# Kernel optimization log

Hardware: AMD Instinct MI355X
Metric: run time of the kernel (lower is better)

Reference implementation:

```python
import jax, jax.numpy as jnp
import numpy as np

N, IN, OUT, RANK = 8192, 4096, 4096, 16
SCALING = 2.0

def setup_inputs() -> dict:
    key = jax.random.key(0)
    k1, k2, k3, k4 = jax.random.split(key, 4)
    x = jax.random.normal(k1, (N, IN), dtype=jnp.float32)
    weight = jax.random.normal(k2, (OUT, IN), dtype=jnp.float32) * (1.0 / np.sqrt(IN))
    lora_A = jax.random.normal(k3, (RANK, IN), dtype=jnp.float32) * (1.0 / np.sqrt(IN))
    lora_B = jax.random.normal(k4, (OUT, RANK), dtype=jnp.float32) * 0.01
    return {"x": x, "weight": weight, "lora_A": lora_A, "lora_B": lora_B}

def reference(x, weight, lora_A, lora_B):
    # frozen base linear: F.linear(x, weight) == x @ weight.T  -> [N, OUT]
    base = jnp.einsum('ni,oi->no', x, weight)
    # LoRA branch: dropout(x) (p=0 => identity) @ A.T @ B.T, scaled
    lora = jnp.einsum('ni,ri->nr', x, lora_A)      # [N, RANK]
    lora = jnp.einsum('nr,or->no', lora, lora_B)   # [N, OUT]
    return base + lora * SCALING
```

## Files before the change

### kernel.cpp

```cpp
#include <hip/hip_runtime.h>


#define N_ROWS 8192
#define K_DIM  4096
#define N_COLS 4096
#define RANK   16
#define BK     64
#define NT     (K_DIM / BK)

#define XBLK ((N_ROWS * K_DIM / 4) / 256)
#define WBLK ((N_COLS * K_DIM / 4) / 256)

typedef __bf16 bf16x8 __attribute__((ext_vector_type(8)));
typedef float  f32x4  __attribute__((ext_vector_type(4)));

__device__ __forceinline__ unsigned short f2bf(float f) {
  unsigned int u = __builtin_bit_cast(unsigned int, f);
  u += 0x7FFFu + ((u >> 16) & 1u);
  return (unsigned short)(u >> 16);
}


__global__ __launch_bounds__(256) void prep_kernel(const float* __restrict__ x,
                                                   const float* __restrict__ w,
                                                   const float* __restrict__ A,
                                                   const float* __restrict__ Bm,
                                                   unsigned short* __restrict__ xb,
                                                   unsigned short* __restrict__ wb) {
  const int b = blockIdx.x;
  if (b < XBLK) {
    size_t idx = (size_t)b * 256 + threadIdx.x;
    const float4 v = *reinterpret_cast<const float4*>(x + idx * 4);
    ushort4 r;
    r.x = f2bf(v.x); r.y = f2bf(v.y); r.z = f2bf(v.z); r.w = f2bf(v.w);
    *reinterpret_cast<ushort4*>(xb + idx * 4) = r;
  } else {
    size_t idx = (size_t)(b - XBLK) * 256 + threadIdx.x;
    int o  = (int)(idx >> 10);
    int ic = (int)(idx & 1023) << 2;
    const float4 wv = *reinterpret_cast<const float4*>(w + (size_t)o * K_DIM + ic);
    float a0 = wv.x, a1 = wv.y, a2 = wv.z, a3 = wv.w;
    float br[RANK];
#pragma unroll
    for (int r4 = 0; r4 < RANK / 4; ++r4) {
      const float4 bv = *reinterpret_cast<const float4*>(Bm + (size_t)o * RANK + r4 * 4);
      br[r4 * 4 + 0] = bv.x; br[r4 * 4 + 1] = bv.y;
      br[r4 * 4 + 2] = bv.z; br[r4 * 4 + 3] = bv.w;
    }
#pragma unroll
    for (int r = 0; r < RANK; ++r) {
      const float4 av = *reinterpret_cast<const float4*>(A + (size_t)r * K_DIM + ic);
      float b2 = br[r] * 2.0f;
      a0 += b2 * av.x; a1 += b2 * av.y; a2 += b2 * av.z; a3 += b2 * av.w;
    }
    ushort4 rr;
    rr.x = f2bf(a0); rr.y = f2bf(a1); rr.z = f2bf(a2); rr.w = f2bf(a3);
    *reinterpret_cast<ushort4*>(wb + (size_t)o * K_DIM + ic) = rr;
  }
}


__device__ __forceinline__ void gload_lds16(const void* g, void* l) {
  __builtin_amdgcn_global_load_lds(
      (__attribute__((address_space(1))) void*)g,
      (__attribute__((address_space(3))) void*)l, 16, 0, 0);
}

__global__ __launch_bounds__(512, 1) void gemm_bf16_r8(
    const unsigned short* __restrict__ xb, const unsigned short* __restrict__ wb,
    float* __restrict__ out) {
  __shared__ __align__(16) char smem[131072];

  const int t  = threadIdx.x;
  const int l  = t & 63;
  const int wv = t >> 6;
  const int lr = l & 15;
  const int lk = l >> 4;
  const int wr = wv >> 2;
  const int wc = wv & 3;

  const int bid  = blockIdx.x;
  const int sbid = (bid & 7) * 64 + (bid >> 3);
  const int bm   = sbid >> 4;
  const int bn   = sbid & 15;

  const int srow = t >> 3;
  const int scol = ((t & 7) ^ ((t >> 3) & 7)) << 3;
  const unsigned short* gA = xb + (size_t)(bm * 256 + srow) * K_DIM + scol;
  const unsigned short* gB = wb + (size_t)(bn * 256 + srow) * K_DIM + scol;
  char* ldsA = smem + t * 16;
  char* ldsB = smem + 65536 + t * 16;

#define STG_A(hh, SRC, NB) do {                                                 \
    const unsigned short* _g = (SRC) + (size_t)((hh) * 128) * K_DIM;            \
    char* _l = ldsA + (NB) + (hh) * 16384;                                      \
    gload_lds16(_g, _l);                                                        \
    gload_lds16(_g + (size_t)64 * K_DIM, _l + 8192);                            \
  } while (0)
#define STG_B(hh, SRC, NB) do {                                                 \
    const unsigned short* _g = (SRC) + (size_t)((hh) * 128) * K_DIM;            \
    char* _l = ldsB + (NB) + (hh) * 16384;                                      \
    gload_lds16(_g, _l);                                                        \
    gload_lds16(_g + (size_t)64 * K_DIM, _l + 8192);                            \
  } while (0)

  const int g0   = (lk ^ (lr & 7)) << 4;
  const int g1   = ((lk + 4) ^ (lr & 7)) << 4;
  const int aoff = (wr * 16 + lr) * 128;
  const int boff = (wc * 16 + lr) * 128;

  bf16x8 aF[8];
  bf16x8 bE[4];
  bf16x8 bO[4];
  f32x4 acc[8][4];
#pragma unroll
  for (int m = 0; m < 8; ++m)
#pragma unroll
    for (int n = 0; n < 4; ++n)
      acc[m][n] = (f32x4){0.f, 0.f, 0.f, 0.f};

#define RD_A(BASE) do {                                                         \
    _Pragma("unroll")                                                           \
    for (int m = 0; m < 4; ++m) {                                               \
      aF[2 * m + 0] = *(const bf16x8*)(smem + (BASE) + m * 4096 + aoff + g0);   \
      aF[2 * m + 1] = *(const bf16x8*)(smem + (BASE) + m * 4096 + aoff + g1);   \
    }                                                                           \
  } while (0)
#define RD_B(DST, BASE) do {                                                    \
    _Pragma("unroll")                                                           \
    for (int n = 0; n < 2; ++n) {                                               \
      DST[2 * n + 0] = *(const bf16x8*)(smem + 65536 + (BASE) + n * 8192 + boff + g0); \
      DST[2 * n + 1] = *(const bf16x8*)(smem + 65536 + (BASE) + n * 8192 + boff + g1); \
    }                                                                           \
  } while (0)

#define MFMA_Q(MB, NB0, BF) do {                                                \
    _Pragma("unroll")                                                           \
    for (int mi = 0; mi < 4; ++mi)                                              \
      _Pragma("unroll")                                                         \
      for (int ni = 0; ni < 2; ++ni)                                            \
        _Pragma("unroll")                                                       \
        for (int kk = 0; kk < 2; ++kk)                                          \
          acc[(MB) + mi][(NB0) + ni] = __builtin_amdgcn_mfma_f32_16x16x32_bf16( \
              aF[mi * 2 + kk], BF[ni * 2 + kk], acc[(MB) + mi][(NB0) + ni], 0, 0, 0); \
  } while (0)

#define TILE(CB, NB, T) do {                                                    \
    const int _t1 = ((T) + 1 < NT) ? (T) + 1 : NT - 1;                          \
    const unsigned short* _sA = gA + (size_t)_t1 * BK;                          \
    const unsigned short* _sB = gB + (size_t)_t1 * BK;                          \
                                     \
    STG_A(0, _sA, NB); STG_A(1, _sA, NB);                                       \
    STG_B(0, _sB, NB); STG_B(1, _sB, NB);                                       \
    __builtin_amdgcn_sched_barrier(0);                                          \
      \
    RD_A((CB));                                                                 \
    RD_B(bE, (CB));                                                             \
    RD_B(bO, (CB) + 16384);                                                     \
    MFMA_Q(0, 0, bE);                                                           \
    MFMA_Q(0, 2, bO);                                                           \
    RD_A((CB) + 16384);                                                         \
    MFMA_Q(4, 0, bE);                                                           \
    MFMA_Q(4, 2, bO);                                                           \
        \
    asm volatile("s_waitcnt lgkmcnt(0)");                                       \
    __builtin_amdgcn_sched_barrier(0);                                          \
    asm volatile("s_waitcnt vmcnt(0)");                                         \
    __builtin_amdgcn_s_barrier();                                               \
    __builtin_amdgcn_sched_barrier(0);                                          \
  } while (0)

  STG_A(0, gA, 0); STG_A(1, gA, 0); STG_B(0, gB, 0); STG_B(1, gB, 0);
  __builtin_amdgcn_sched_barrier(0);
  asm volatile("s_waitcnt vmcnt(0)");
  __builtin_amdgcn_s_barrier();
  __builtin_amdgcn_sched_barrier(0);

#pragma nounroll
  for (int u = 0; u < NT / 2; ++u) {
    TILE(0, 32768, 2 * u);
    TILE(32768, 0, 2 * u + 1);
  }

  const int orow = bm * 256 + wr * 16 + lk * 4;
  const int ocol = bn * 256 + wc * 16 + lr;
#pragma unroll
  for (int mf = 0; mf < 8; ++mf)
#pragma unroll
    for (int nf = 0; nf < 4; ++nf)
#pragma unroll
      for (int j = 0; j < 4; ++j)
        out[(size_t)(orow + mf * 32 + j) * N_COLS + (ocol + nf * 64)] = acc[mf][nf][j];

#undef STG_A
#undef STG_B
#undef RD_A
#undef RD_B
#undef MFMA_Q
#undef TILE
}


__global__ __launch_bounds__(256) void fallback_kernel(const float* __restrict__ x,
                                                       const float* __restrict__ w,
                                                       const float* __restrict__ A,
                                                       const float* __restrict__ Bm,
                                                       float* __restrict__ out) {
  const int o    = blockIdx.x * 256 + threadIdx.x;
  const int nrow = blockIdx.y;
  float bro[RANK];
#pragma unroll
  for (int r = 0; r < RANK; ++r) bro[r] = Bm[(size_t)o * RANK + r] * 2.0f;
  float bacc = 0.f;
  float tacc[RANK];
#pragma unroll
  for (int r = 0; r < RANK; ++r) tacc[r] = 0.f;
  for (int k = 0; k < K_DIM; ++k) {
    float xv = x[(size_t)nrow * K_DIM + k];
    bacc += xv * w[(size_t)o * K_DIM + k];
#pragma unroll
    for (int r = 0; r < RANK; ++r) tacc[r] += xv * A[(size_t)r * K_DIM + k];
  }
  float res = bacc;
#pragma unroll
  for (int r = 0; r < RANK; ++r) res += bro[r] * tacc[r];
  out[(size_t)nrow * N_COLS + o] = res;
}


extern "C" void kernel_launch(void* const* d_in, const int* in_sizes, int n_in,
                              void* d_out, int out_size, void* d_ws, size_t ws_size,
                              hipStream_t stream) {
  const float* x  = (const float*)d_in[0];
  const float* w  = (const float*)d_in[1];
  const float* A  = (const float*)d_in[2];
  const float* Bm = (const float*)d_in[3];
  float* out = (float*)d_out;

  const size_t need = ((size_t)N_ROWS * K_DIM + (size_t)N_COLS * K_DIM) * sizeof(unsigned short);
  if (ws_size < need) {
    dim3 grid(N_COLS / 256, N_ROWS);
    fallback_kernel<<<grid, 256, 0, stream>>>(x, w, A, Bm, out);
    return;
  }

  unsigned short* xb = (unsigned short*)d_ws;
  unsigned short* wb = xb + (size_t)N_ROWS * K_DIM;

  prep_kernel<<<XBLK + WBLK, 256, 0, stream>>>(x, w, A, Bm, xb, wb);

  const int grid_gemm = (N_ROWS / 256) * (N_COLS / 256);
  gemm_bf16_r8<<<grid_gemm, 512, 0, stream>>>(xb, wb, out);
}
```

Before: 310.0 us.

## Use four-stage LDS ring with BK=32 and register double-buffered fragments

New measurement: 325.3 us. 5.0% more time.

```diff
diff --git a/kernel.cpp b/kernel.cpp
--- a/kernel.cpp
+++ b/kernel.cpp
@@ -5,7 +5,7 @@
 #define K_DIM  4096
 #define N_COLS 4096
 #define RANK   16
-#define BK     64
+#define BK     32
 #define NT     (K_DIM / BK)
 
 #define XBLK ((N_ROWS * K_DIM / 4) / 256)
@@ -66,7 +66,7 @@
       (__attribute__((address_space(3))) void*)l, 16, 0, 0);
 }
 
-__global__ __launch_bounds__(512, 1) void gemm_bf16_r8(
+__global__ __launch_bounds__(512, 1) void gemm_bf16_r10(
     const unsigned short* __restrict__ xb, const unsigned short* __restrict__ wb,
     float* __restrict__ out) {
   __shared__ __align__(16) char smem[131072];
@@ -84,34 +84,30 @@
   const int bm   = sbid >> 4;
   const int bn   = sbid & 15;
 
-  const int srow = t >> 3;
-  const int scol = ((t & 7) ^ ((t >> 3) & 7)) << 3;
-  const unsigned short* gA = xb + (size_t)(bm * 256 + srow) * K_DIM + scol;
-  const unsigned short* gB = wb + (size_t)(bn * 256 + srow) * K_DIM + scol;
-  char* ldsA = smem + t * 16;
-  char* ldsB = smem + 65536 + t * 16;
-
-#define STG_A(hh, SRC, NB) do {                                                 \
-    const unsigned short* _g = (SRC) + (size_t)((hh) * 128) * K_DIM;            \
-    char* _l = ldsA + (NB) + (hh) * 16384;                                      \
+  const int slog  = (t & 7) ^ ((t >> 3) & 7);
+  const int s_row = 2 * (t >> 3) + (slog >> 2);
+  const int s_k   = (slog & 3) * 8;
+  const unsigned short* gA = xb + (size_t)(bm * 256 + s_row) * K_DIM + s_k;
+  const unsigned short* gB = wb + (size_t)(bn * 256 + s_row) * K_DIM + s_k;
+
+#define STG_A(BUFB, KT) do {                                                    \
+    const unsigned short* _g = gA + (size_t)(KT) * BK;                          \
+    char* _l = smem + (BUFB) + t * 16;                                          \
     gload_lds16(_g, _l);                                                        \
-    gload_lds16(_g + (size_t)64 * K_DIM, _l + 8192);                            \
-  } while (0)
-#define STG_B(hh, SRC, NB) do {                                                 \
-    const unsigned short* _g = (SRC) + (size_t)((hh) * 128) * K_DIM;            \
-    char* _l = ldsB + (NB) + (hh) * 16384;                                      \
+    gload_lds16(_g + (size_t)128 * K_DIM, _l + 8192);                           \
+  } while (0)
+#define STG_B(BUFB, KT) do {                                                    \
+    const unsigned short* _g = gB + (size_t)(KT) * BK;                          \
+    char* _l = smem + (BUFB) + 16384 + t * 16;                                  \
     gload_lds16(_g, _l);                                                        \
-    gload_lds16(_g + (size_t)64 * K_DIM, _l + 8192);                            \
-  } while (0)
-
-  const int g0   = (lk ^ (lr & 7)) << 4;
-  const int g1   = ((lk + 4) ^ (lr & 7)) << 4;
-  const int aoff = (wr * 16 + lr) * 128;
-  const int boff = (wc * 16 + lr) * 128;
-
-  bf16x8 aF[8];
-  bf16x8 bE[4];
-  bf16x8 bO[4];
+    gload_lds16(_g + (size_t)128 * K_DIM, _l + 8192);                           \
+  } while (0)
+
+  const int lane_off = (lr >> 1) * 128 + (((((lr & 1) << 2) | lk) ^ (lr >> 1)) << 4);
+  const int a_base = wr * 1024 + lane_off;
+  const int b_base = 16384 + wc * 1024 + lane_off;
+
+  bf16x8 sA0[8], sB0[4], sA1[8], sB1[4];
   f32x4 acc[8][4];
 #pragma unroll
   for (int m = 0; m < 8; ++m)
@@ -119,67 +115,53 @@
     for (int n = 0; n < 4; ++n)
       acc[m][n] = (f32x4){0.f, 0.f, 0.f, 0.f};
 
-#define RD_A(BASE) do {                                                         \
+#define RD_SET(SA, SB, RB) do {                                                 \
     _Pragma("unroll")                                                           \
-    for (int m = 0; m < 4; ++m) {                                               \
-      aF[2 * m + 0] = *(const bf16x8*)(smem + (BASE) + m * 4096 + aoff + g0);   \
-      aF[2 * m + 1] = *(const bf16x8*)(smem + (BASE) + m * 4096 + aoff + g1);   \
-    }                                                                           \
-  } while (0)
-#define RD_B(DST, BASE) do {                                                    \
+    for (int m = 0; m < 8; ++m)                                                 \
+      SA[m] = *(const bf16x8*)(smem + (RB) + a_base + m * 2048);                \
     _Pragma("unroll")                                                           \
-    for (int n = 0; n < 2; ++n) {                                               \
-      DST[2 * n + 0] = *(const bf16x8*)(smem + 65536 + (BASE) + n * 8192 + boff + g0); \
-      DST[2 * n + 1] = *(const bf16x8*)(smem + 65536 + (BASE) + n * 8192 + boff + g1); \
-    }                                                                           \
-  } while (0)
-
-#define MFMA_Q(MB, NB0, BF) do {                                                \
+    for (int n = 0; n < 4; ++n)                                                 \
+      SB[n] = *(const bf16x8*)(smem + (RB) + b_base + n * 4096);                \
+  } while (0)
+
+#define MF_SET(SA, SB) do {                                                     \
     _Pragma("unroll")                                                           \
-    for (int mi = 0; mi < 4; ++mi)                                              \
+    for (int m = 0; m < 8; ++m)                                                 \
       _Pragma("unroll")                                                         \
-      for (int ni = 0; ni < 2; ++ni)                                            \
-        _Pragma("unroll")                                                       \
-        for (int kk = 0; kk < 2; ++kk)                                          \
-          acc[(MB) + mi][(NB0) + ni] = __builtin_amdgcn_mfma_f32_16x16x32_bf16( \
-              aF[mi * 2 + kk], BF[ni * 2 + kk], acc[(MB) + mi][(NB0) + ni], 0, 0, 0); \
-  } while (0)
-
-#define TILE(CB, NB, T) do {                                                    \
-    const int _t1 = ((T) + 1 < NT) ? (T) + 1 : NT - 1;                          \
-    const unsigned short* _sA = gA + (size_t)_t1 * BK;                          \
-    const unsigned short* _sB = gB + (size_t)_t1 * BK;                          \
-                                     \
-    STG_A(0, _sA, NB); STG_A(1, _sA, NB);                                       \
-    STG_B(0, _sB, NB); STG_B(1, _sB, NB);                                       \
+      for (int n = 0; n < 4; ++n)                                               \
+        acc[m][n] = __builtin_amdgcn_mfma_f32_16x16x32_bf16(                    \
+            SA[m], SB[n], acc[m][n], 0, 0, 0);                                  \
+  } while (0)
+
+#define BODY(RB_OFF, SB_OFF, CUR_A, CUR_B, NXT_A, NXT_B, TT) do {               \
+    const int _ts = ((TT) + 3 < NT) ? (TT) + 3 : NT - 1;                        \
+    STG_A(SB_OFF, _ts); STG_B(SB_OFF, _ts);                                     \
+    RD_SET(NXT_A, NXT_B, RB_OFF);                                               \
+    __builtin_amdgcn_s_setprio(1);                                              \
+    MF_SET(CUR_A, CUR_B);                                                       \
+    __builtin_amdgcn_s_setprio(0);                                              \
     __builtin_amdgcn_sched_barrier(0);                                          \
-      \
-    RD_A((CB));                                                                 \
-    RD_B(bE, (CB));                                                             \
-    RD_B(bO, (CB) + 16384);                                                     \
-    MFMA_Q(0, 0, bE);                                                           \
-    MFMA_Q(0, 2, bO);                                                           \
-    RD_A((CB) + 16384);                                                         \
-    MFMA_Q(4, 0, bE);                                                           \
-    MFMA_Q(4, 2, bO);                                                           \
-        \
-    asm volatile("s_waitcnt lgkmcnt(0)");                                       \
-    __builtin_amdgcn_sched_barrier(0);                                          \
-    asm volatile("s_waitcnt vmcnt(0)");                                         \
+    asm volatile("s_waitcnt vmcnt(4)");                                         \
     __builtin_amdgcn_s_barrier();                                               \
     __builtin_amdgcn_sched_barrier(0);                                          \
   } while (0)
 
-  STG_A(0, gA, 0); STG_A(1, gA, 0); STG_B(0, gB, 0); STG_B(1, gB, 0);
+  STG_A(0, 0);      STG_B(0, 0);
+  STG_A(32768, 1);  STG_B(32768, 1);
+  STG_A(65536, 2);  STG_B(65536, 2);
   __builtin_amdgcn_sched_barrier(0);
-  asm volatile("s_waitcnt vmcnt(0)");
+  asm volatile("s_waitcnt vmcnt(4)");
   __builtin_amdgcn_s_barrier();
   __builtin_amdgcn_sched_barrier(0);
+  RD_SET(sA0, sB0, 0);
 
 #pragma nounroll
-  for (int u = 0; u < NT / 2; ++u) {
-    TILE(0, 32768, 2 * u);
-    TILE(32768, 0, 2 * u + 1);
+  for (int u = 0; u < NT / 4; ++u) {
+    const int tb = 4 * u;
+    BODY(32768, 98304, sA0, sB0, sA1, sB1, tb);
+    BODY(65536, 0,     sA1, sB1, sA0, sB0, tb + 1);
+    BODY(98304, 32768, sA0, sB0, sA1, sB1, tb + 2);
+    BODY(0,     65536, sA1, sB1, sA0, sB0, tb + 3);
   }
 
   const int orow = bm * 256 + wr * 16 + lk * 4;
@@ -194,10 +176,9 @@
 
 #undef STG_A
 #undef STG_B
-#undef RD_A
-#undef RD_B
-#undef MFMA_Q
-#undef TILE
+#undef RD_SET
+#undef MF_SET
+#undef BODY
 }
 
 
@@ -250,5 +231,5 @@
   prep_kernel<<<XBLK + WBLK, 256, 0, stream>>>(x, w, A, Bm, xb, wb);
 
   const int grid_gemm = (N_ROWS / 256) * (N_COLS / 256);
-  gemm_bf16_r8<<<grid_gemm, 512, 0, stream>>>(xb, wb, out);
-}
+  gemm_bf16_r10<<<grid_gemm, 512, 0, stream>>>(xb, wb, out);
+}
```

## Restructure GEMM main loop into interleaved load/MFMA phases with partial vmcnt waits

Applied to the files above, without the earlier changes.

After: 536.1 us. 1.73x slower.

```diff
diff --git a/kernel.cpp b/kernel.cpp
--- a/kernel.cpp
+++ b/kernel.cpp
@@ -66,7 +66,7 @@
       (__attribute__((address_space(3))) void*)l, 16, 0, 0);
 }
 
-__global__ __launch_bounds__(512, 1) void gemm_bf16_r8(
+__global__ __launch_bounds__(512, 1) void gemm_bf16_r13(
     const unsigned short* __restrict__ xb, const unsigned short* __restrict__ wb,
     float* __restrict__ out) {
   __shared__ __align__(16) char smem[131072];
@@ -88,20 +88,11 @@
   const int scol = ((t & 7) ^ ((t >> 3) & 7)) << 3;
   const unsigned short* gA = xb + (size_t)(bm * 256 + srow) * K_DIM + scol;
   const unsigned short* gB = wb + (size_t)(bn * 256 + srow) * K_DIM + scol;
-  char* ldsA = smem + t * 16;
-  char* ldsB = smem + 65536 + t * 16;
-
-#define STG_A(hh, SRC, NB) do {                                                 \
-    const unsigned short* _g = (SRC) + (size_t)((hh) * 128) * K_DIM;            \
-    char* _l = ldsA + (NB) + (hh) * 16384;                                      \
-    gload_lds16(_g, _l);                                                        \
-    gload_lds16(_g + (size_t)64 * K_DIM, _l + 8192);                            \
-  } while (0)
-#define STG_B(hh, SRC, NB) do {                                                 \
-    const unsigned short* _g = (SRC) + (size_t)((hh) * 128) * K_DIM;            \
-    char* _l = ldsB + (NB) + (hh) * 16384;                                      \
-    gload_lds16(_g, _l);                                                        \
-    gload_lds16(_g + (size_t)64 * K_DIM, _l + 8192);                            \
+
+#define STG_HALF(OFF, SRC) do {                                                 \
+    char* _l = smem + (OFF) + t * 16;                                           \
+    gload_lds16((SRC), _l);                                                     \
+    gload_lds16((SRC) + (size_t)64 * K_DIM, _l + 8192);                         \
   } while (0)
 
   const int g0   = (lk ^ (lr & 7)) << 4;
@@ -109,9 +100,7 @@
   const int aoff = (wr * 16 + lr) * 128;
   const int boff = (wc * 16 + lr) * 128;
 
-  bf16x8 aF[8];
-  bf16x8 bE[4];
-  bf16x8 bO[4];
+  bf16x8 a0[8], a1[8], b0[4], b1[4];
   f32x4 acc[8][4];
 #pragma unroll
   for (int m = 0; m < 8; ++m)
@@ -119,22 +108,22 @@
     for (int n = 0; n < 4; ++n)
       acc[m][n] = (f32x4){0.f, 0.f, 0.f, 0.f};
 
-#define RD_A(BASE) do {                                                         \
+#define RD_A(DST, BASE) do {                                                    \
     _Pragma("unroll")                                                           \
     for (int m = 0; m < 4; ++m) {                                               \
-      aF[2 * m + 0] = *(const bf16x8*)(smem + (BASE) + m * 4096 + aoff + g0);   \
-      aF[2 * m + 1] = *(const bf16x8*)(smem + (BASE) + m * 4096 + aoff + g1);   \
+      DST[2 * m + 0] = *(const bf16x8*)(smem + (BASE) + m * 4096 + aoff + g0);  \
+      DST[2 * m + 1] = *(const bf16x8*)(smem + (BASE) + m * 4096 + aoff + g1);  \
     }                                                                           \
   } while (0)
 #define RD_B(DST, BASE) do {                                                    \
     _Pragma("unroll")                                                           \
     for (int n = 0; n < 2; ++n) {                                               \
-      DST[2 * n + 0] = *(const bf16x8*)(smem + 65536 + (BASE) + n * 8192 + boff + g0); \
-      DST[2 * n + 1] = *(const bf16x8*)(smem + 65536 + (BASE) + n * 8192 + boff + g1); \
+      DST[2 * n + 0] = *(const bf16x8*)(smem + (BASE) + n * 8192 + boff + g0);  \
+      DST[2 * n + 1] = *(const bf16x8*)(smem + (BASE) + n * 8192 + boff + g1);  \
     }                                                                           \
   } while (0)
 
-#define MFMA_Q(MB, NB0, BF) do {                                                \
+#define MFMA_Q(MB, AF, NB0, BF) do {                                            \
     _Pragma("unroll")                                                           \
     for (int mi = 0; mi < 4; ++mi)                                              \
       _Pragma("unroll")                                                         \
@@ -142,44 +131,74 @@
         _Pragma("unroll")                                                       \
         for (int kk = 0; kk < 2; ++kk)                                          \
           acc[(MB) + mi][(NB0) + ni] = __builtin_amdgcn_mfma_f32_16x16x32_bf16( \
-              aF[mi * 2 + kk], BF[ni * 2 + kk], acc[(MB) + mi][(NB0) + ni], 0, 0, 0); \
-  } while (0)
-
-#define TILE(CB, NB, T) do {                                                    \
-    const int _t1 = ((T) + 1 < NT) ? (T) + 1 : NT - 1;                          \
-    const unsigned short* _sA = gA + (size_t)_t1 * BK;                          \
-    const unsigned short* _sB = gB + (size_t)_t1 * BK;                          \
-                                     \
-    STG_A(0, _sA, NB); STG_A(1, _sA, NB);                                       \
-    STG_B(0, _sB, NB); STG_B(1, _sB, NB);                                       \
-    __builtin_amdgcn_sched_barrier(0);                                          \
-      \
-    RD_A((CB));                                                                 \
-    RD_B(bE, (CB));                                                             \
-    RD_B(bO, (CB) + 16384);                                                     \
-    MFMA_Q(0, 0, bE);                                                           \
-    MFMA_Q(0, 2, bO);                                                           \
-    RD_A((CB) + 16384);                                                         \
-    MFMA_Q(4, 0, bE);                                                           \
-    MFMA_Q(4, 2, bO);                                                           \
-        \
+              AF[mi * 2 + kk], BF[ni * 2 + kk], acc[(MB) + mi][(NB0) + ni], 0, 0, 0); \
+  } while (0)
+
+#define PH_PRE() do {                                                           \
+    __builtin_amdgcn_sched_barrier(0);                                          \
+    __builtin_amdgcn_s_barrier();                                               \
     asm volatile("s_waitcnt lgkmcnt(0)");                                       \
     __builtin_amdgcn_sched_barrier(0);                                          \
-    asm volatile("s_waitcnt vmcnt(0)");                                         \
+    __builtin_amdgcn_s_setprio(1);                                              \
+  } while (0)
+#define PH_POST() do {                                                          \
+    __builtin_amdgcn_s_setprio(0);                                              \
+    __builtin_amdgcn_sched_barrier(0);                                          \
     __builtin_amdgcn_s_barrier();                                               \
     __builtin_amdgcn_sched_barrier(0);                                          \
   } while (0)
-
-  STG_A(0, gA, 0); STG_A(1, gA, 0); STG_B(0, gB, 0); STG_B(1, gB, 0);
+#define PH_POST_VM6() do {                                                      \
+    __builtin_amdgcn_s_setprio(0);                                              \
+    __builtin_amdgcn_sched_barrier(0);                                          \
+    asm volatile("s_waitcnt vmcnt(6)");                                         \
+    __builtin_amdgcn_s_barrier();                                               \
+    __builtin_amdgcn_sched_barrier(0);                                          \
+  } while (0)
+
+#define GROUP(RB, OB, T) do {                                                   \
+    const int _ts = ((T) + 2 < NT) ? (T) + 2 : NT - 1;                          \
+    const unsigned short* _sA = gA + (size_t)_ts * BK;                          \
+    const unsigned short* _sB = gB + (size_t)_ts * BK;                          \
+                                    \
+    RD_B(b0, (RB) + 32768);                                                     \
+    RD_B(b1, (RB) + 49152);                                                     \
+    STG_HALF((RB) + 0, _sA);                                                    \
+    PH_PRE(); MFMA_Q(0, a0, 0, b0); PH_POST();                                  \
+                                       \
+    RD_A(a1, (RB) + 16384);                                                     \
+    STG_HALF((RB) + 32768, _sB);                                                \
+    PH_PRE(); MFMA_Q(0, a0, 2, b1); PH_POST();                                  \
+                          \
+    RD_A(a0, (OB) + 0);                                                         \
+    STG_HALF((RB) + 16384, _sA + (size_t)128 * K_DIM);                          \
+    PH_PRE(); MFMA_Q(4, a1, 2, b1); PH_POST();                                  \
+                                       \
+    STG_HALF((RB) + 49152, _sB + (size_t)128 * K_DIM);                          \
+    PH_PRE(); MFMA_Q(4, a1, 0, b0); PH_POST_VM6();                              \
+  } while (0)
+
+  STG_HALF(0,     gA);
+  STG_HALF(16384, gA + (size_t)128 * K_DIM);
+  STG_HALF(32768, gB);
+  STG_HALF(49152, gB + (size_t)128 * K_DIM);
+  {
+    const unsigned short* g1A = gA + (size_t)BK;
+    const unsigned short* g1B = gB + (size_t)BK;
+    STG_HALF(65536 + 0,     g1A);
+    STG_HALF(65536 + 16384, g1A + (size_t)128 * K_DIM);
+    STG_HALF(65536 + 32768, g1B);
+    STG_HALF(65536 + 49152, g1B + (size_t)128 * K_DIM);
+  }
   __builtin_amdgcn_sched_barrier(0);
   asm volatile("s_waitcnt vmcnt(0)");
   __builtin_amdgcn_s_barrier();
   __builtin_amdgcn_sched_barrier(0);
+  RD_A(a0, 0);
 
 #pragma nounroll
   for (int u = 0; u < NT / 2; ++u) {
-    TILE(0, 32768, 2 * u);
-    TILE(32768, 0, 2 * u + 1);
+    GROUP(0,     65536, 2 * u);
+    GROUP(65536, 0,     2 * u + 1);
   }
 
   const int orow = bm * 256 + wr * 16 + lk * 4;
@@ -192,12 +211,14 @@
       for (int j = 0; j < 4; ++j)
         out[(size_t)(orow + mf * 32 + j) * N_COLS + (ocol + nf * 64)] = acc[mf][nf][j];
 
-#undef STG_A
-#undef STG_B
+#undef STG_HALF
 #undef RD_A
 #undef RD_B
 #undef MFMA_Q
-#undef TILE
+#undef PH_PRE
+#undef PH_POST
+#undef PH_POST_VM6
+#undef GROUP
 }
 
 
@@ -250,5 +271,5 @@
   prep_kernel<<<XBLK + WBLK, 256, 0, stream>>>(x, w, A, Bm, xb, wb);
 
   const int grid_gemm = (N_ROWS / 256) * (N_COLS / 256);
-  gemm_bf16_r8<<<grid_gemm, 512, 0, stream>>>(xb, wb, out);
-}
+  gemm_bf16_r13<<<grid_gemm, 512, 0, stream>>>(xb, wb, out);
+}
```

## Switch GEMM to 32x32x16 MFMA with 4x2 wave tiling

Applied to the files above, without the earlier changes.

New measurement: 346.2 us. +11.7%, slower.

```diff
diff --git a/kernel.cpp b/kernel.cpp
--- a/kernel.cpp
+++ b/kernel.cpp
@@ -12,7 +12,7 @@
 #define WBLK ((N_COLS * K_DIM / 4) / 256)
 
 typedef __bf16 bf16x8 __attribute__((ext_vector_type(8)));
-typedef float  f32x4  __attribute__((ext_vector_type(4)));
+typedef float  f32x16 __attribute__((ext_vector_type(16)));
 
 __device__ __forceinline__ unsigned short f2bf(float f) {
   unsigned int u = __builtin_bit_cast(unsigned int, f);
@@ -66,18 +66,18 @@
       (__attribute__((address_space(3))) void*)l, 16, 0, 0);
 }
 
-__global__ __launch_bounds__(512, 1) void gemm_bf16_r8(
+__global__ __launch_bounds__(512, 1) void gemm_bf16_r14(
     const unsigned short* __restrict__ xb, const unsigned short* __restrict__ wb,
     float* __restrict__ out) {
   __shared__ __align__(16) char smem[131072];
 
-  const int t  = threadIdx.x;
-  const int l  = t & 63;
-  const int wv = t >> 6;
-  const int lr = l & 15;
-  const int lk = l >> 4;
-  const int wr = wv >> 2;
-  const int wc = wv & 3;
+  const int t   = threadIdx.x;
+  const int l   = t & 63;
+  const int wv  = t >> 6;
+  const int l31 = l & 31;
+  const int l5  = l >> 5;
+  const int wm  = wv >> 1;
+  const int wn  = wv & 1;
 
   const int bid  = blockIdx.x;
   const int sbid = (bid & 7) * 64 + (bid >> 3);
@@ -104,45 +104,55 @@
     gload_lds16(_g + (size_t)64 * K_DIM, _l + 8192);                            \
   } while (0)
 
-  const int g0   = (lk ^ (lr & 7)) << 4;
-  const int g1   = ((lk + 4) ^ (lr & 7)) << 4;
-  const int aoff = (wr * 16 + lr) * 128;
-  const int boff = (wc * 16 + lr) * 128;
+  const int gr0 = ((0 + l5) ^ (l31 & 7)) << 4;
+  const int gr1 = ((2 + l5) ^ (l31 & 7)) << 4;
+  const int gr2 = ((4 + l5) ^ (l31 & 7)) << 4;
+  const int gr3 = ((6 + l5) ^ (l31 & 7)) << 4;
+  const int a_base = (wm >> 1) * 16384 + (wm & 1) * 8192 + l31 * 128;
+  const int b_base = 65536 + wn * 16384 + l31 * 128;
 
   bf16x8 aF[8];
-  bf16x8 bE[4];
-  bf16x8 bO[4];
-  f32x4 acc[8][4];
-#pragma unroll
-  for (int m = 0; m < 8; ++m)
+  bf16x8 bF[16];
+  f32x16 acc[2][4];
+#pragma unroll
+  for (int m = 0; m < 2; ++m)
 #pragma unroll
     for (int n = 0; n < 4; ++n)
-      acc[m][n] = (f32x4){0.f, 0.f, 0.f, 0.f};
-
-#define RD_A(BASE) do {                                                         \
+#pragma unroll
+      for (int e = 0; e < 16; ++e)
+        acc[m][n][e] = 0.f;
+
+#define RD_A(CB_) do {                                                          \
     _Pragma("unroll")                                                           \
-    for (int m = 0; m < 4; ++m) {                                               \
-      aF[2 * m + 0] = *(const bf16x8*)(smem + (BASE) + m * 4096 + aoff + g0);   \
-      aF[2 * m + 1] = *(const bf16x8*)(smem + (BASE) + m * 4096 + aoff + g1);   \
+    for (int m = 0; m < 2; ++m) {                                               \
+      const char* _p = smem + (CB_) + a_base + m * 4096;                        \
+      aF[4 * m + 0] = *(const bf16x8*)(_p + gr0);                               \
+      aF[4 * m + 1] = *(const bf16x8*)(_p + gr1);                               \
+      aF[4 * m + 2] = *(const bf16x8*)(_p + gr2);                               \
+      aF[4 * m + 3] = *(const bf16x8*)(_p + gr3);                               \
     }                                                                           \
   } while (0)
-#define RD_B(DST, BASE) do {                                                    \
+#define RD_B2(NF0, CB_) do {                                                    \
     _Pragma("unroll")                                                           \
     for (int n = 0; n < 2; ++n) {                                               \
-      DST[2 * n + 0] = *(const bf16x8*)(smem + 65536 + (BASE) + n * 8192 + boff + g0); \
-      DST[2 * n + 1] = *(const bf16x8*)(smem + 65536 + (BASE) + n * 8192 + boff + g1); \
+      const char* _p = smem + (CB_) + b_base + ((NF0) + n) * 4096;              \
+      bF[4 * ((NF0) + n) + 0] = *(const bf16x8*)(_p + gr0);                     \
+      bF[4 * ((NF0) + n) + 1] = *(const bf16x8*)(_p + gr1);                     \
+      bF[4 * ((NF0) + n) + 2] = *(const bf16x8*)(_p + gr2);                     \
+      bF[4 * ((NF0) + n) + 3] = *(const bf16x8*)(_p + gr3);                     \
     }                                                                           \
   } while (0)
 
-#define MFMA_Q(MB, NB0, BF) do {                                                \
+#define MFMA_N2(NF0) do {                                                       \
     _Pragma("unroll")                                                           \
-    for (int mi = 0; mi < 4; ++mi)                                              \
+    for (int mi = 0; mi < 2; ++mi)                                              \
       _Pragma("unroll")                                                         \
       for (int ni = 0; ni < 2; ++ni)                                            \
         _Pragma("unroll")                                                       \
-        for (int kk = 0; kk < 2; ++kk)                                          \
-          acc[(MB) + mi][(NB0) + ni] = __builtin_amdgcn_mfma_f32_16x16x32_bf16( \
-              aF[mi * 2 + kk], BF[ni * 2 + kk], acc[(MB) + mi][(NB0) + ni], 0, 0, 0); \
+        for (int kk = 0; kk < 4; ++kk)                                          \
+          acc[mi][(NF0) + ni] = __builtin_amdgcn_mfma_f32_32x32x16_bf16(        \
+              aF[mi * 4 + kk], bF[4 * ((NF0) + ni) + kk],                       \
+              acc[mi][(NF0) + ni], 0, 0, 0);                                    \
   } while (0)
 
 #define TILE(CB, NB, T) do {                                                    \
@@ -155,13 +165,10 @@
     __builtin_amdgcn_sched_barrier(0);                                          \
       \
     RD_A((CB));                                                                 \
-    RD_B(bE, (CB));                                                             \
-    RD_B(bO, (CB) + 16384);                                                     \
-    MFMA_Q(0, 0, bE);                                                           \
-    MFMA_Q(0, 2, bO);                                                           \
-    RD_A((CB) + 16384);                                                         \
-    MFMA_Q(4, 0, bE);                                                           \
-    MFMA_Q(4, 2, bO);                                                           \
+    RD_B2(0, (CB));                                                             \
+    MFMA_N2(0);                                                                 \
+    RD_B2(2, (CB));                                                             \
+    MFMA_N2(2);                                                                 \
         \
     asm volatile("s_waitcnt lgkmcnt(0)");                                       \
     __builtin_amdgcn_sched_barrier(0);                                          \
@@ -182,21 +189,23 @@
     TILE(32768, 0, 2 * u + 1);
   }
 
-  const int orow = bm * 256 + wr * 16 + lk * 4;
-  const int ocol = bn * 256 + wc * 16 + lr;
-#pragma unroll
-  for (int mf = 0; mf < 8; ++mf)
+  const int orow = bm * 256 + wm * 64 + l5 * 4;
+  const int ocol = bn * 256 + wn * 128 + l31;
+#pragma unroll
+  for (int mf = 0; mf < 2; ++mf)
 #pragma unroll
     for (int nf = 0; nf < 4; ++nf)
 #pragma unroll
-      for (int j = 0; j < 4; ++j)
-        out[(size_t)(orow + mf * 32 + j) * N_COLS + (ocol + nf * 64)] = acc[mf][nf][j];
+      for (int reg = 0; reg < 16; ++reg) {
+        const int row = orow + mf * 32 + (reg & 3) + 8 * (reg >> 2);
+        out[(size_t)row * N_COLS + (ocol + nf * 32)] = acc[mf][nf][reg];
+      }
 
 #undef STG_A
 #undef STG_B
 #undef RD_A
-#undef RD_B
-#undef MFMA_Q
+#undef RD_B2
+#undef MFMA_N2
 #undef TILE
 }
 
@@ -250,5 +259,5 @@
   prep_kernel<<<XBLK + WBLK, 256, 0, stream>>>(x, w, A, Bm, xb, wb);
 
   const int grid_gemm = (N_ROWS / 256) * (N_COLS / 256);
-  gemm_bf16_r8<<<grid_gemm, 512, 0, stream>>>(xb, wb, out);
-}
+  gemm_bf16_r14<<<grid_gemm, 512, 0, stream>>>(xb, wb, out);
+}
```
